# Optimization experiments

Measured on AMD Instinct MI355X. Metric: run time of the kernel, lower is better.

## Reference

```python
import jax, jax.numpy as jnp
import numpy as np
from jax import lax

CLASSNUM = 10575
IN_FEATS = 512
MARGIN = 0.2
SCALE = 32.0
EPS_SECOND = 0.0001


def setup_inputs() -> dict:
    key = jax.random.key(0)
    k1, k2, k3 = jax.random.split(key, 3)
    B = 4096
    x = jax.random.normal(k1, (B, IN_FEATS), dtype=jnp.float32)
    label = jax.random.randint(k2, (B,), 0, CLASSNUM, dtype=jnp.int64)
    # xavier_uniform init for weight [classnum, in_feats]
    limit = float(np.sqrt(6.0 / (CLASSNUM + IN_FEATS)))
    weight = jax.random.uniform(k3, (CLASSNUM, IN_FEATS), dtype=jnp.float32,
                                minval=-limit, maxval=limit)
    return {"x": x, "label": label, "weight": weight}


def _l2_normalize(v, axis=-1):
    # matches F.normalize(p=2, eps=1e-12)
    n = jnp.linalg.norm(v, axis=axis, keepdims=True)
    return v / jnp.maximum(n, 1e-12)


def reference(x, label, weight):
    label = label.astype(jnp.int32)
    # cos_theta: [B, classnum]
    cos_theta = jnp.clip(_l2_normalize(x) @ _l2_normalize(weight).T, -1.0, 1.0)
    B = x.shape[0]
    rows = jnp.arange(B)
    cosin_simi = cos_theta[rows, label][:, None]  # [B,1]

    # softmax stats used only to pick rival index (detached in torch)
    soft = lax.stop_gradient(jax.nn.softmax(cos_theta, axis=1))
    max_index = jnp.argmax(soft, axis=1)                      # [B]
    max_num = soft[rows, max_index][:, None]                  # [B,1]
    masked = jnp.where(soft < max_num - EPS_SECOND, soft, 0.0)
    second_index = jnp.argmax(masked, axis=1)                 # [B]
    rival_index = jnp.where(max_index == label, second_index, max_index)
    rival_cosin_simi = lax.stop_gradient(cos_theta[rows, rival_index][:, None])

    # cosface, easy_margin=True
    score = jnp.where(cosin_simi > 0, cosin_simi - MARGIN, cosin_simi)
    rival_score = jnp.where(rival_cosin_simi > 0.6,
                            (rival_cosin_simi + MARGIN) * 0.2,
                            rival_cosin_simi)

    out = cos_theta.at[rows, rival_index].set(rival_score[:, 0])
    out = out.at[rows, label].set(score[:, 0])
    return out * SCALE
```

## Files before the change

kernel.cpp:

```cpp
#include <hip/hip_runtime.h>
#include <stdint.h>
#include <math.h>

#define CLASSNUM 10575
#define NPAD     10752
#define BATCH    4096
#define KDIM     512
#define BK       64
#define MARGIN   0.2f
#define SCALE    32.0f
#define EPS2     1.0e-4f
#define FLAG_THR 0.58f

typedef __bf16 bf16_t;
typedef __attribute__((ext_vector_type(8))) __bf16 bf16x8;
typedef __attribute__((ext_vector_type(4))) float f32x4;

__device__ __forceinline__ unsigned short f2bf(float f) {
  union { float f; unsigned u; } v; v.f = f;
  return (unsigned short)((v.u + 0x7FFFu + ((v.u >> 16) & 1u)) >> 16);
}

__device__ __forceinline__ void async_ld16(const void* g, void* lds) {
  __builtin_amdgcn_global_load_lds(
      (__attribute__((address_space(1))) void*)(const_cast<void*>(g)),
      (__attribute__((address_space(3))) void*)lds, 16, 0, 0);
}

__global__ __launch_bounds__(256) void normalize_rows_bf16(
    const float* __restrict__ src, unsigned short* __restrict__ dst,
    int nrows, int nrows_pad) {
  int row  = blockIdx.x * 4 + (threadIdx.x >> 6);
  int lane = threadIdx.x & 63;
  if (row >= nrows_pad) return;
  unsigned short o[8] = {0,0,0,0,0,0,0,0};
  if (row < nrows) {
    const float4* rp = (const float4*)(src + (size_t)row * KDIM);
    float4 a = rp[lane * 2 + 0];
    float4 b = rp[lane * 2 + 1];
    float ss = a.x*a.x + a.y*a.y + a.z*a.z + a.w*a.w
             + b.x*b.x + b.y*b.y + b.z*b.z + b.w*b.w;
    #pragma unroll
    for (int off = 32; off > 0; off >>= 1) ss += __shfl_xor(ss, off, 64);
    float rn = 1.0f / fmaxf(sqrtf(ss), 1e-12f);
    o[0]=f2bf(a.x*rn); o[1]=f2bf(a.y*rn); o[2]=f2bf(a.z*rn); o[3]=f2bf(a.w*rn);
    o[4]=f2bf(b.x*rn); o[5]=f2bf(b.y*rn); o[6]=f2bf(b.z*rn); o[7]=f2bf(b.w*rn);
  }
  ushort4* dp = (ushort4*)(dst + (size_t)row * KDIM);
  dp[lane*2+0] = make_ushort4(o[0],o[1],o[2],o[3]);
  dp[lane*2+1] = make_ushort4(o[4],o[5],o[6],o[7]);
}

__global__ __launch_bounds__(256) void label_cos_kernel(
    const float* __restrict__ x, const float* __restrict__ w,
    const int* __restrict__ label, float* __restrict__ cls,
    float* __restrict__ score32, unsigned* __restrict__ flags) {
  int row  = blockIdx.x * 4 + (threadIdx.x >> 6);
  int lane = threadIdx.x & 63;
  if (row >= BATCH) return;
  int l = label[row];
  const float4* xp = (const float4*)(x + (size_t)row * KDIM);
  const float4* wp = (const float4*)(w + (size_t)l * KDIM);
  float dxx = 0.f, dww = 0.f, dxw = 0.f;
  #pragma unroll
  for (int i = 0; i < 2; ++i) {
    float4 a = xp[lane*2+i];
    float4 b = wp[lane*2+i];
    dxx += a.x*a.x + a.y*a.y + a.z*a.z + a.w*a.w;
    dww += b.x*b.x + b.y*b.y + b.z*b.z + b.w*b.w;
    dxw += a.x*b.x + a.y*b.y + a.z*b.z + a.w*b.w;
  }
  #pragma unroll
  for (int off = 32; off > 0; off >>= 1) {
    dxx += __shfl_xor(dxx, off, 64);
    dww += __shfl_xor(dww, off, 64);
    dxw += __shfl_xor(dxw, off, 64);
  }
  if (lane == 0) {
    float c = dxw / (fmaxf(sqrtf(dxx), 1e-12f) * fmaxf(sqrtf(dww), 1e-12f));
    c = fminf(fmaxf(c, -1.0f), 1.0f);
    cls[row] = c;
    score32[row] = SCALE * ((c > 0.0f) ? (c - MARGIN) : c);
    flags[row] = 0u;
  }
}

__global__ __launch_bounds__(512) void gemm_bf16(
    const bf16_t* __restrict__ A,
    const bf16_t* __restrict__ Bm,
    float* __restrict__ out, unsigned* __restrict__ flags,
    const int* __restrict__ label, const float* __restrict__ score32) {
  __shared__ bf16_t As[256 * BK];
  __shared__ bf16_t Bs[256 * BK];

  const int bm = blockIdx.x, bn = blockIdx.y;
  const int tid = threadIdx.x, lane = tid & 63, wave = tid >> 6;
  const int waveM = wave >> 2, waveN = wave & 3;

  const f32x4 z4 = {0.f, 0.f, 0.f, 0.f};
  f32x4 acc[8][4];
  #pragma unroll
  for (int i = 0; i < 8; ++i)
    #pragma unroll
    for (int j = 0; j < 4; ++j) acc[i][j] = z4;

  const int srow = tid >> 3;
  const int scg  = (tid & 7) ^ (srow & 7);
  const bf16_t* agB = A  + (size_t)(bm * 256 + srow) * KDIM + scg * 8;
  const bf16_t* bgB = Bm + (size_t)(bn * 256 + srow) * KDIM + scg * 8;

  const int fr  = lane & 15;
  const int fq  = lane >> 4;
  const int psw = lane & 7;

  #pragma unroll 1
  for (int kt = 0; kt < KDIM / BK; ++kt) {
    const int kb = kt * BK;
    #pragma unroll
    for (int R = 0; R < 4; ++R)
      async_ld16(agB + (size_t)(R * 64) * KDIM + kb,
                 (char*)As + R * 8192 + wave * 1024);
    #pragma unroll
    for (int R = 0; R < 4; ++R)
      async_ld16(bgB + (size_t)(R * 64) * KDIM + kb,
                 (char*)Bs + R * 8192 + wave * 1024);
    __syncthreads();

    #pragma unroll
    for (int ksub = 0; ksub < 2; ++ksub) {
      const int q = ksub * 4 + fq;
      const int p = q ^ psw;
      bf16x8 af[8], bfr[4];
      #pragma unroll
      for (int i = 0; i < 8; ++i) {
        int r = waveM * 128 + i * 16 + fr;
        af[i] = *(const bf16x8*)(As + r * BK + p * 8);
      }
      #pragma unroll
      for (int i = 0; i < 4; ++i) {
        int r = waveN * 64 + i * 16 + fr;
        bfr[i] = *(const bf16x8*)(Bs + r * BK + p * 8);
      }
      #pragma unroll
      for (int mi = 0; mi < 8; ++mi)
        #pragma unroll
        for (int ni = 0; ni < 4; ++ni)
          acc[mi][ni] = __builtin_amdgcn_mfma_f32_16x16x32_bf16(
              af[mi], bfr[ni], acc[mi][ni], 0, 0, 0);
    }
    __syncthreads();
  }

  int*   labL   = (int*)As;
  float* scoreL = (float*)((char*)As + 1024);
  if (tid < 256) {
    labL[tid]   = label[bm * 256 + tid];
    scoreL[tid] = score32[bm * 256 + tid];
  }
  __syncthreads();

  const int colBase = bn * 256 + waveN * 64 + fr;
  #pragma unroll
  for (int mi = 0; mi < 8; ++mi) {
    #pragma unroll
    for (int r = 0; r < 4; ++r) {
      int rloc = waveM * 128 + mi * 16 + fq * 4 + r;
      int row  = bm * 256 + rloc;
      int lab  = labL[rloc];
      float sc = scoreL[rloc];
      float mx = -2.0f;
      #pragma unroll
      for (int ni = 0; ni < 4; ++ni) {
        int col = colBase + ni * 16;
        float v = fminf(fmaxf(acc[mi][ni][r], -1.0f), 1.0f);
        mx = fmaxf(mx, v);
        float vs = (col == lab) ? sc : SCALE * v;
        if (col < CLASSNUM) out[(size_t)row * CLASSNUM + col] = vs;
      }
      if (mx > FLAG_THR) atomicOr(flags + row, 1u);
    }
  }
}

__global__ __launch_bounds__(256) void fixup_kernel(
    float* __restrict__ out, const int* __restrict__ label,
    const float* __restrict__ cls, const unsigned* __restrict__ flags) {
  const int row  = blockIdx.x * 4 + (threadIdx.x >> 6);
  const int lane = threadIdx.x & 63;
  if (flags[row] == 0u) return;

  float* orow = out + (size_t)row * CLASSNUM;
  const int lab = label[row];
  const float labv = SCALE * cls[row];

  float bv = -1e30f; int bi = 0;
  for (int i = lane; i < CLASSNUM; i += 64) {
    float v = (i == lab) ? labv : orow[i];
    if (v > bv) { bv = v; bi = i; }
  }
  #pragma unroll
  for (int off = 32; off > 0; off >>= 1) {
    float ov = __shfl_xor(bv, off, 64);
    int   oi = __shfl_xor(bi, off, 64);
    if (ov > bv || (ov == bv && oi < bi)) { bv = ov; bi = oi; }
  }
  const float cmax = bv * (1.0f / 32.0f);
  const int maxIdx = bi;

  float zz = 0.f;
  for (int i = lane; i < CLASSNUM; i += 64) {
    float v = (i == lab) ? labv : orow[i];
    zz += expf(v * (1.0f / 32.0f) - cmax);
  }
  #pragma unroll
  for (int off = 32; off > 0; off >>= 1) zz += __shfl_xor(zz, off, 64);
  const float Z = zz;
  const float thr = 1.0f / Z - EPS2;

  float mbv = -1.0f; int mbi = 0;
  for (int i = lane; i < CLASSNUM; i += 64) {
    float v = (i == lab) ? labv : orow[i];
    float soft = expf(v * (1.0f / 32.0f) - cmax) / Z;
    float m = (soft < thr) ? soft : 0.0f;
    if (m > mbv) { mbv = m; mbi = i; }
  }
  #pragma unroll
  for (int off = 32; off > 0; off >>= 1) {
    float ov = __shfl_xor(mbv, off, 64);
    int   oi = __shfl_xor(mbi, off, 64);
    if (ov > mbv || (ov == mbv && oi < mbi)) { mbv = ov; mbi = oi; }
  }

  if (lane == 0) {
    int rival = (maxIdx == lab) ? mbi : maxIdx;
    float rc  = ((rival == lab) ? labv : orow[rival]) * (1.0f / 32.0f);
    float rs  = (rc > 0.6f) ? (rc + MARGIN) * 0.2f : rc;
    orow[rival] = SCALE * rs;
    float cl = cls[row];
    float scv = (cl > 0.0f) ? (cl - MARGIN) : cl;
    orow[lab] = SCALE * scv;
  }
}

extern "C" void kernel_launch(void* const* d_in, const int* in_sizes, int n_in,
                              void* d_out, int out_size, void* d_ws, size_t ws_size,
                              hipStream_t stream) {
  const float* x     = (const float*)d_in[0];
  const int*   label = (const int*)d_in[1];
  const float* w     = (const float*)d_in[2];
  float* out = (float*)d_out;

  unsigned short* xn = (unsigned short*)d_ws;
  unsigned short* wn = xn + (size_t)BATCH * KDIM;
  float* cls     = (float*)(wn + (size_t)NPAD * KDIM);
  float* score32 = cls + BATCH;
  unsigned* flags = (unsigned*)(score32 + BATCH);

  normalize_rows_bf16<<<BATCH / 4, 256, 0, stream>>>(x, xn, BATCH, BATCH);
  normalize_rows_bf16<<<NPAD / 4, 256, 0, stream>>>(w, wn, CLASSNUM, NPAD);
  label_cos_kernel<<<BATCH / 4, 256, 0, stream>>>(x, w, label, cls,
                                                  score32, flags);

  dim3 g(BATCH / 256, NPAD / 256);
  gemm_bf16<<<g, 512, 0, stream>>>((const bf16_t*)xn, (const bf16_t*)wn,
                                   out, flags, label, score32);

  fixup_kernel<<<BATCH / 4, 256, 0, stream>>>(out, label, cls, flags);
}
```

Measured before the change: 254.2 us.

## Triple-buffer GEMM K-loop with async LDS prefetch and smaller N tile

Changes the GEMM tile from 256x256 to 256x128, so the grid has twice as many blocks and each wave holds a 4x4 accumulator set instead of 8x4. The K loop now uses a three-stage LDS ring buffer, prefetching tiles two steps ahead in halves interleaved with fragment loads, and waits with explicit vmcnt and barriers. MFMA bursts are wrapped in s_setprio. The aim is to hide global-load latency, raise occupancy and cut register pressure, at the cost of more total loads of the x tile and more LDS per block.

```diff
diff --git a/kernel.cpp b/kernel.cpp
--- a/kernel.cpp
+++ b/kernel.cpp
@@ -6,7 +6,10 @@
 #define NPAD     10752
 #define BATCH    4096
 #define KDIM     512
+#define BM       256
+#define BN       128
 #define BK       64
+#define NKT      (KDIM / BK)
 #define MARGIN   0.2f
 #define SCALE    32.0f
 #define EPS2     1.0e-4f
@@ -85,87 +88,125 @@
   }
 }
 
+
+#define ABUF_B 32768
+#define BBUF_B 16384
+#define BUF_B  (ABUF_B + BBUF_B)
+
+struct Frags { bf16x8 a[4]; bf16x8 b[4]; };
+
+__device__ __forceinline__ Frags ld_frags(const char* base, int ksub,
+                                          int waveM, int waveN,
+                                          int fr, int fq) {
+  Frags f;
+  const bf16_t* Ab = (const bf16_t*)base;
+  const bf16_t* Bb = (const bf16_t*)(base + ABUF_B);
+  const int q = ksub * 4 + fq;
+  const int p = (q ^ (fr & 7)) * 8;
+  #pragma unroll
+  for (int i = 0; i < 4; ++i) {
+    int ra = waveM * 64 + i * 16 + fr;
+    f.a[i] = *(const bf16x8*)(Ab + ra * BK + p);
+    int rb = waveN * 64 + i * 16 + fr;
+    f.b[i] = *(const bf16x8*)(Bb + rb * BK + p);
+  }
+  return f;
+}
+
+__device__ __forceinline__ void mfma16(const Frags& f, f32x4 (&acc)[4][4]) {
+  __builtin_amdgcn_s_setprio(1);
+  #pragma unroll
+  for (int mi = 0; mi < 4; ++mi)
+    #pragma unroll
+    for (int ni = 0; ni < 4; ++ni)
+      acc[mi][ni] = __builtin_amdgcn_mfma_f32_16x16x32_bf16(
+          f.a[mi], f.b[ni], acc[mi][ni], 0, 0, 0);
+  __builtin_amdgcn_s_setprio(0);
+}
+
 __global__ __launch_bounds__(512) void gemm_bf16(
     const bf16_t* __restrict__ A,
     const bf16_t* __restrict__ Bm,
     float* __restrict__ out, unsigned* __restrict__ flags,
     const int* __restrict__ label, const float* __restrict__ score32) {
-  __shared__ bf16_t As[256 * BK];
-  __shared__ bf16_t Bs[256 * BK];
+  __shared__ __align__(16) char lds[3 * BUF_B];
 
   const int bm = blockIdx.x, bn = blockIdx.y;
   const int tid = threadIdx.x, lane = tid & 63, wave = tid >> 6;
-  const int waveM = wave >> 2, waveN = wave & 3;
+  const int waveM = wave >> 1, waveN = wave & 1;
 
   const f32x4 z4 = {0.f, 0.f, 0.f, 0.f};
-  f32x4 acc[8][4];
-  #pragma unroll
-  for (int i = 0; i < 8; ++i)
+  f32x4 acc[4][4];
+  #pragma unroll
+  for (int i = 0; i < 4; ++i)
     #pragma unroll
     for (int j = 0; j < 4; ++j) acc[i][j] = z4;
 
   const int srow = tid >> 3;
   const int scg  = (tid & 7) ^ (srow & 7);
-  const bf16_t* agB = A  + (size_t)(bm * 256 + srow) * KDIM + scg * 8;
-  const bf16_t* bgB = Bm + (size_t)(bn * 256 + srow) * KDIM + scg * 8;
-
-  const int fr  = lane & 15;
-  const int fq  = lane >> 4;
-  const int psw = lane & 7;
+  const bf16_t* agB = A  + (size_t)(bm * BM + srow) * KDIM + scg * 8;
+  const bf16_t* bgB = Bm + (size_t)(bn * BN + srow) * KDIM + scg * 8;
+
+  const int fr = lane & 15;
+  const int fq = lane >> 4;
+
+  auto stage = [&](int t, int part) {
+    char* base = lds + (t % 3) * BUF_B;
+    const int kb = t * BK;
+    const int Ra = part * 2;
+    async_ld16(agB + (size_t)(Ra * 64) * KDIM + kb,
+               base + Ra * 8192 + wave * 1024);
+    async_ld16(agB + (size_t)((Ra + 1) * 64) * KDIM + kb,
+               base + (Ra + 1) * 8192 + wave * 1024);
+    async_ld16(bgB + (size_t)(part * 64) * KDIM + kb,
+               base + ABUF_B + part * 8192 + wave * 1024);
+  };
+
+  stage(0, 0); stage(0, 1);
+  stage(1, 0); stage(1, 1);
 
   #pragma unroll 1
-  for (int kt = 0; kt < KDIM / BK; ++kt) {
-    const int kb = kt * BK;
-    #pragma unroll
-    for (int R = 0; R < 4; ++R)
-      async_ld16(agB + (size_t)(R * 64) * KDIM + kb,
-                 (char*)As + R * 8192 + wave * 1024);
-    #pragma unroll
-    for (int R = 0; R < 4; ++R)
-      async_ld16(bgB + (size_t)(R * 64) * KDIM + kb,
-                 (char*)Bs + R * 8192 + wave * 1024);
-    __syncthreads();
-
-    #pragma unroll
-    for (int ksub = 0; ksub < 2; ++ksub) {
-      const int q = ksub * 4 + fq;
-      const int p = q ^ psw;
-      bf16x8 af[8], bfr[4];
-      #pragma unroll
-      for (int i = 0; i < 8; ++i) {
-        int r = waveM * 128 + i * 16 + fr;
-        af[i] = *(const bf16x8*)(As + r * BK + p * 8);
-      }
-      #pragma unroll
-      for (int i = 0; i < 4; ++i) {
-        int r = waveN * 64 + i * 16 + fr;
-        bfr[i] = *(const bf16x8*)(Bs + r * BK + p * 8);
-      }
-      #pragma unroll
-      for (int mi = 0; mi < 8; ++mi)
-        #pragma unroll
-        for (int ni = 0; ni < 4; ++ni)
-          acc[mi][ni] = __builtin_amdgcn_mfma_f32_16x16x32_bf16(
-              af[mi], bfr[ni], acc[mi][ni], 0, 0, 0);
-    }
-    __syncthreads();
-  }
-
-  int*   labL   = (int*)As;
-  float* scoreL = (float*)((char*)As + 1024);
+  for (int t = 0; t < NKT - 1; ++t) {
+    asm volatile("s_waitcnt vmcnt(6)" ::: "memory");
+    asm volatile("s_barrier" ::: "memory");
+    const char* base = lds + (t % 3) * BUF_B;
+
+    Frags f0 = ld_frags(base, 0, waveM, waveN, fr, fq);
+    if (t < NKT - 2) stage(t + 2, 0);
+    asm volatile("s_barrier" ::: "memory");
+    mfma16(f0, acc);
+
+    Frags f1 = ld_frags(base, 1, waveM, waveN, fr, fq);
+    if (t < NKT - 2) stage(t + 2, 1);
+    asm volatile("s_barrier" ::: "memory");
+    mfma16(f1, acc);
+  }
+  {
+    asm volatile("s_waitcnt vmcnt(0)" ::: "memory");
+    asm volatile("s_barrier" ::: "memory");
+    const char* base = lds + ((NKT - 1) % 3) * BUF_B;
+    Frags f0 = ld_frags(base, 0, waveM, waveN, fr, fq);
+    mfma16(f0, acc);
+    Frags f1 = ld_frags(base, 1, waveM, waveN, fr, fq);
+    mfma16(f1, acc);
+  }
+
+  __syncthreads();
+  int*   labL   = (int*)lds;
+  float* scoreL = (float*)(lds + 1024);
   if (tid < 256) {
-    labL[tid]   = label[bm * 256 + tid];
-    scoreL[tid] = score32[bm * 256 + tid];
+    labL[tid]   = label[bm * BM + tid];
+    scoreL[tid] = score32[bm * BM + tid];
   }
   __syncthreads();
 
-  const int colBase = bn * 256 + waveN * 64 + fr;
-  #pragma unroll
-  for (int mi = 0; mi < 8; ++mi) {
+  const int colBase = bn * BN + waveN * 64 + fr;
+  #pragma unroll
+  for (int mi = 0; mi < 4; ++mi) {
     #pragma unroll
     for (int r = 0; r < 4; ++r) {
-      int rloc = waveM * 128 + mi * 16 + fq * 4 + r;
-      int row  = bm * 256 + rloc;
+      int rloc = waveM * 64 + mi * 16 + fq * 4 + r;
+      int row  = bm * BM + rloc;
       int lab  = labL[rloc];
       float sc = scoreL[rloc];
       float mx = -2.0f;
@@ -261,7 +302,7 @@
   label_cos_kernel<<<BATCH / 4, 256, 0, stream>>>(x, w, label, cls,
                                                   score32, flags);
 
-  dim3 g(BATCH / 256, NPAD / 256);
+  dim3 g(BATCH / BM, NPAD / BN);
   gemm_bf16<<<g, 512, 0, stream>>>((const bf16_t*)xn, (const bf16_t*)wn,
                                    out, flags, label, score32);
 
```

New measurement: 253.0 us. Within noise of the previous version (-0.5%).
